# Optimization experiments

Hardware: AMD Instinct MI355X
Metric: run time of the kernel (lower is better)

## Reference

```python
import jax, jax.numpy as jnp
import numpy as np

SCALE = 1.0 / np.sqrt(128.0)  # 1/sqrt(D)


def setup_inputs() -> dict:
    key = jax.random.key(0)
    kq, kk, kv = jax.random.split(key, 3)
    B, Sq, Sk, D = 32, 2048, 2048, 128
    q = jax.random.normal(kq, (B, Sq, D), dtype=jnp.float32)
    k = jax.random.normal(kk, (B, Sk, D), dtype=jnp.float32)
    v = jax.random.normal(kv, (B, Sk, D), dtype=jnp.float32)
    return {"q": q, "k": k, "v": v}


def reference(q, k, v):
    # attention = bmm(q, k^T) * scale  -> [B, Sq, Sk]
    attention = jnp.einsum("bqd,bkd->bqk", q, k) * SCALE
    # no mask (attn_mask=None path); softmax over last dim (dim=2)
    attention = jax.nn.softmax(attention, axis=2)
    # dropout p=0.0 is identity at eval
    context = jnp.einsum("bqk,bkd->bqd", attention, v)  # [B, Sq, D]
    return (context, attention)
```

## Files before the change

kernel.cpp:

```cpp
#include <hip/hip_runtime.h>
#include <hip/hip_bf16.h>


#define B_  32
#define SQ  2048
#define SK  2048
#define DD  128
#define SCALE 0.08838834764831845f

using short8   = __attribute__((ext_vector_type(8))) short;
using ushort4t = __attribute__((ext_vector_type(4))) unsigned short;
using f32x4    = __attribute__((ext_vector_type(4))) float;

#define K_OFF 0
#define K_RS  272
#define V_OFF 8704
#define V_RS  80
#define P_OFF 18944
#define P_RS  80
#define LDS_BYTES 24064

__device__ __forceinline__ unsigned short f2bf(float f) {
  union { float f; unsigned u; } a; a.f = f;
  unsigned r = a.u + 0x7FFFu + ((a.u >> 16) & 1u);
  return (unsigned short)(r >> 16);
}

__global__ __launch_bounds__(256, 4)
void attn_fwd(const float* __restrict__ q, const float* __restrict__ k,
              const float* __restrict__ v, float* __restrict__ out) {
  __shared__ float4 smem_v[LDS_BYTES / 16];
  char* smem = (char*)smem_v;

  const int t  = threadIdx.x;
  const int w  = t >> 6;
  const int l  = t & 63;
  const int lr = l & 15;
  const int lg = l >> 4;
  const int qt = blockIdx.x;
  const int b  = blockIdx.y;
  const int q0 = qt * 64 + w * 16;

  short8 qf[4];
  {
    const float* qg = q + ((size_t)b * SQ + q0 + lr) * DD;
#pragma unroll
    for (int kk = 0; kk < 4; ++kk) {
      const int d0 = kk * 32 + lg * 8;
      float4 x = *(const float4*)(qg + d0);
      float4 y = *(const float4*)(qg + d0 + 4);
      short8 f;
      f[0] = (short)f2bf(x.x * SCALE); f[1] = (short)f2bf(x.y * SCALE);
      f[2] = (short)f2bf(x.z * SCALE); f[3] = (short)f2bf(x.w * SCALE);
      f[4] = (short)f2bf(y.x * SCALE); f[5] = (short)f2bf(y.y * SCALE);
      f[6] = (short)f2bf(y.z * SCALE); f[7] = (short)f2bf(y.w * SCALE);
      qf[kk] = f;
    }
  }

  f32x4 ctx[8];
#pragma unroll
  for (int i = 0; i < 8; ++i) ctx[i] = (f32x4){0.f, 0.f, 0.f, 0.f};
  float lsum[4] = {0.f, 0.f, 0.f, 0.f};

  char* const pl = smem + P_OFF + w * (16 * P_RS);

#pragma unroll 1
  for (int kt = 0; kt < SK / 32; ++kt) {
    const int kb = kt * 32;
    __syncthreads();
#pragma unroll
    for (int i = 0; i < 4; ++i) {
      int u = i * 256 + t;
      int row = u >> 5, c4 = u & 31;
      float4 kv = *(const float4*)(k + ((size_t)b * SK + kb + row) * DD + c4 * 4);
      ushort4t o = {f2bf(kv.x), f2bf(kv.y), f2bf(kv.z), f2bf(kv.w)};
      *(ushort4t*)(smem + K_OFF + row * K_RS + c4 * 8) = o;
    }
#pragma unroll
    for (int i = 0; i < 4; ++i) {
      int u = i * 256 + t;
      int d = u & 127, kq = u >> 7;
      const float* vp = v + ((size_t)b * SK + kb + kq * 4) * DD + d;
      ushort4t o = {f2bf(vp[0]), f2bf(vp[DD]), f2bf(vp[2 * DD]), f2bf(vp[3 * DD])};
      *(ushort4t*)(smem + V_OFF + d * V_RS + kq * 8) = o;
    }
    __syncthreads();

    f32x4 s0 = {0.f, 0.f, 0.f, 0.f}, s1 = {0.f, 0.f, 0.f, 0.f};
#pragma unroll
    for (int kk = 0; kk < 4; ++kk) {
      short8 b0 = *(const short8*)(smem + K_OFF + lr * K_RS + kk * 64 + lg * 16);
      short8 b1 = *(const short8*)(smem + K_OFF + (16 + lr) * K_RS + kk * 64 + lg * 16);
      s0 = __builtin_amdgcn_mfma_f32_16x16x32_bf16(qf[kk], b0, s0, 0, 0, 0);
      s1 = __builtin_amdgcn_mfma_f32_16x16x32_bf16(qf[kk], b1, s1, 0, 0, 0);
    }

#pragma unroll
    for (int ri = 0; ri < 4; ++ri) {
      float e0 = __expf(s0[ri]);
      float e1 = __expf(s1[ri]);
      lsum[ri] += e0 + e1;
      int prow = lg * 4 + ri;
      *(unsigned short*)(pl + prow * P_RS + lr * 2)        = f2bf(e0);
      *(unsigned short*)(pl + prow * P_RS + (16 + lr) * 2) = f2bf(e1);
    }
    short8 pa = *(const short8*)(pl + lr * P_RS + lg * 16);
#pragma unroll
    for (int nd = 0; nd < 8; ++nd) {
      short8 vb = *(const short8*)(smem + V_OFF + (nd * 16 + lr) * V_RS + lg * 16);
      ctx[nd] = __builtin_amdgcn_mfma_f32_16x16x32_bf16(pa, vb, ctx[nd], 0, 0, 0);
    }
  }

#pragma unroll
  for (int ri = 0; ri < 4; ++ri) {
#pragma unroll
    for (int off = 1; off < 16; off <<= 1)
      lsum[ri] += __shfl_xor(lsum[ri], off, 64);
  }
  float rinv[4];
#pragma unroll
  for (int ri = 0; ri < 4; ++ri) rinv[ri] = 1.0f / lsum[ri];

  {
    float* co = out + ((size_t)b * SQ + q0) * DD;
#pragma unroll
    for (int nd = 0; nd < 8; ++nd)
#pragma unroll
      for (int ri = 0; ri < 4; ++ri) {
        int row = lg * 4 + ri;
        co[(size_t)row * DD + nd * 16 + lr] = ctx[nd][ri] * rinv[ri];
      }
  }

  float* ao = out + (size_t)B_ * SQ * DD + ((size_t)b * SQ + q0) * SK;
#pragma unroll 1
  for (int kt = 0; kt < SK / 32; ++kt) {
    const int kb = kt * 32;
    __syncthreads();
#pragma unroll
    for (int i = 0; i < 4; ++i) {
      int u = i * 256 + t;
      int row = u >> 5, c4 = u & 31;
      float4 kv = *(const float4*)(k + ((size_t)b * SK + kb + row) * DD + c4 * 4);
      ushort4t o = {f2bf(kv.x), f2bf(kv.y), f2bf(kv.z), f2bf(kv.w)};
      *(ushort4t*)(smem + K_OFF + row * K_RS + c4 * 8) = o;
    }
    __syncthreads();

    f32x4 s0 = {0.f, 0.f, 0.f, 0.f}, s1 = {0.f, 0.f, 0.f, 0.f};
#pragma unroll
    for (int kk = 0; kk < 4; ++kk) {
      short8 b0 = *(const short8*)(smem + K_OFF + lr * K_RS + kk * 64 + lg * 16);
      short8 b1 = *(const short8*)(smem + K_OFF + (16 + lr) * K_RS + kk * 64 + lg * 16);
      s0 = __builtin_amdgcn_mfma_f32_16x16x32_bf16(qf[kk], b0, s0, 0, 0, 0);
      s1 = __builtin_amdgcn_mfma_f32_16x16x32_bf16(qf[kk], b1, s1, 0, 0, 0);
    }
#pragma unroll
    for (int ri = 0; ri < 4; ++ri) {
      float p0 = __expf(s0[ri]) * rinv[ri];
      float p1 = __expf(s1[ri]) * rinv[ri];
      int row = lg * 4 + ri;
      ao[(size_t)row * SK + kb + lr]      = p0;
      ao[(size_t)row * SK + kb + 16 + lr] = p1;
    }
  }
}

extern "C" void kernel_launch(void* const* d_in, const int* in_sizes, int n_in,
                              void* d_out, int out_size, void* d_ws, size_t ws_size,
                              hipStream_t stream) {
  const float* q = (const float*)d_in[0];
  const float* k = (const float*)d_in[1];
  const float* v = (const float*)d_in[2];
  float* out = (float*)d_out;
  dim3 grid(SQ / 64, B_, 1);
  attn_fwd<<<grid, 256, 0, stream>>>(q, k, v, out);
}
```

Baseline: 891.3 us.

## Precompute bf16 swizzled Q/K/V in workspace and double-buffer async LDS loads

Adds a prep kernel that converts Q (pre-scaled), K and V to bf16 once and stores K and V in a tile-major, XOR-swizzled layout in the workspace. Without it, every query block re-reads and re-converts the fp32 K and V. The main kernel now streams tiles with global_load_lds into double-buffered LDS, which overlaps loads with MFMA work and removes one barrier per iteration. It also remaps block IDs to group blocks of the same batch, widens the second pass to 64-key tiles, and stages the probability tile through LDS to issue coalesced float4 stores. The cost is an extra kernel launch, workspace traffic and more LDS use per block.

```diff
diff --git a/kernel.cpp b/kernel.cpp
--- a/kernel.cpp
+++ b/kernel.cpp
@@ -8,17 +8,15 @@
 #define DD  128
 #define SCALE 0.08838834764831845f
 
-using short8   = __attribute__((ext_vector_type(8))) short;
-using ushort4t = __attribute__((ext_vector_type(4))) unsigned short;
-using f32x4    = __attribute__((ext_vector_type(4))) float;
-
-#define K_OFF 0
-#define K_RS  272
-#define V_OFF 8704
-#define V_RS  80
-#define P_OFF 18944
-#define P_RS  80
-#define LDS_BYTES 24064
+#define WSQ_OFF 0u
+#define WSK_OFF (16u << 20)
+#define WSV_OFF (32u << 20)
+
+using short8 = __attribute__((ext_vector_type(8))) short;
+using f32x4  = __attribute__((ext_vector_type(4))) float;
+
+typedef const __attribute__((address_space(1))) unsigned int* gp_t;
+typedef __attribute__((address_space(3))) unsigned int* sp_t;
 
 __device__ __forceinline__ unsigned short f2bf(float f) {
   union { float f; unsigned u; } a; a.f = f;
@@ -26,36 +24,77 @@
   return (unsigned short)(r >> 16);
 }
 
+__device__ __forceinline__ void gl16(const char* g, char* s) {
+  __builtin_amdgcn_global_load_lds((gp_t)g, (sp_t)s, 16, 0, 0);
+}
+
+__global__ void prep(const float* __restrict__ q, const float* __restrict__ k,
+                     const float* __restrict__ v, char* __restrict__ ws) {
+  const int id = blockIdx.x;
+  const int t  = threadIdx.x;
+  if (id < 4096) {
+    size_t u = (size_t)id * 256 + t;
+    const float* src = q + u * 8;
+    float4 a = *(const float4*)src, c = *(const float4*)(src + 4);
+    short8 o;
+    o[0] = (short)f2bf(a.x * SCALE); o[1] = (short)f2bf(a.y * SCALE);
+    o[2] = (short)f2bf(a.z * SCALE); o[3] = (short)f2bf(a.w * SCALE);
+    o[4] = (short)f2bf(c.x * SCALE); o[5] = (short)f2bf(c.y * SCALE);
+    o[6] = (short)f2bf(c.z * SCALE); o[7] = (short)f2bf(c.w * SCALE);
+    *(short8*)(ws + WSQ_OFF + u * 16) = o;
+  } else if (id < 8192) {
+    size_t u = (size_t)(id - 4096) * 256 + t;
+    int c = u & 15, s = (u >> 4) & 2047, b = u >> 15;
+    const float* src = k + ((size_t)b * SQ + s) * DD + c * 8;
+    float4 a = *(const float4*)src, d = *(const float4*)(src + 4);
+    short8 o;
+    o[0] = (short)f2bf(a.x); o[1] = (short)f2bf(a.y);
+    o[2] = (short)f2bf(a.z); o[3] = (short)f2bf(a.w);
+    o[4] = (short)f2bf(d.x); o[5] = (short)f2bf(d.y);
+    o[6] = (short)f2bf(d.z); o[7] = (short)f2bf(d.w);
+    size_t idx = (size_t)(b * 64 + (s >> 5)) * 512 + (s & 31) * 16 + (c ^ (s & 7));
+    *(short8*)(ws + WSK_OFF + idx * 16) = o;
+  } else {
+    size_t u = (size_t)(id - 8192) * 256 + t;
+    int c = u & 3, d = (u >> 2) & 127, tile = (u >> 9) & 63, b = u >> 15;
+    const float* src = v + ((size_t)b * SK + tile * 32 + c * 8) * DD + d;
+    short8 o;
+#pragma unroll
+    for (int j = 0; j < 8; ++j) o[j] = (short)f2bf(src[(size_t)j * DD]);
+    size_t idx = (size_t)(b * 64 + tile) * 512 + d * 4 + (c ^ (d & 3));
+    *(short8*)(ws + WSV_OFF + idx * 16) = o;
+  }
+}
+
+#define LDS_BYTES 40960
+
 __global__ __launch_bounds__(256, 4)
-void attn_fwd(const float* __restrict__ q, const float* __restrict__ k,
-              const float* __restrict__ v, float* __restrict__ out) {
-  __shared__ float4 smem_v[LDS_BYTES / 16];
-  char* smem = (char*)smem_v;
+void attn_main(const char* __restrict__ ws, float* __restrict__ out) {
+  __shared__ __align__(16) char smem[LDS_BYTES];
 
   const int t  = threadIdx.x;
   const int w  = t >> 6;
   const int l  = t & 63;
   const int lr = l & 15;
   const int lg = l >> 4;
-  const int qt = blockIdx.x;
-  const int b  = blockIdx.y;
+
+  const int orig = blockIdx.x;
+  const int wgid = (orig & 7) * 128 + (orig >> 3);
+  const int b  = wgid >> 5;
+  const int qt = wgid & 31;
   const int q0 = qt * 64 + w * 16;
 
+  const char* wsQ = ws + WSQ_OFF;
+  const char* kt_base = ws + WSK_OFF + (size_t)(b * 64) * 8192;
+  const char* vt_base = ws + WSV_OFF + (size_t)(b * 64) * 8192;
+  char* const scr = smem + 32768 + w * 2048;
+
   short8 qf[4];
   {
-    const float* qg = q + ((size_t)b * SQ + q0 + lr) * DD;
-#pragma unroll
-    for (int kk = 0; kk < 4; ++kk) {
-      const int d0 = kk * 32 + lg * 8;
-      float4 x = *(const float4*)(qg + d0);
-      float4 y = *(const float4*)(qg + d0 + 4);
-      short8 f;
-      f[0] = (short)f2bf(x.x * SCALE); f[1] = (short)f2bf(x.y * SCALE);
-      f[2] = (short)f2bf(x.z * SCALE); f[3] = (short)f2bf(x.w * SCALE);
-      f[4] = (short)f2bf(y.x * SCALE); f[5] = (short)f2bf(y.y * SCALE);
-      f[6] = (short)f2bf(y.z * SCALE); f[7] = (short)f2bf(y.w * SCALE);
-      qf[kk] = f;
-    }
+    const char* qrow = wsQ + ((size_t)b * SQ + q0 + lr) * 256;
+#pragma unroll
+    for (int kk = 0; kk < 4; ++kk)
+      qf[kk] = *(const short8*)(qrow + kk * 64 + lg * 16);
   }
 
   f32x4 ctx[8];
@@ -63,54 +102,57 @@
   for (int i = 0; i < 8; ++i) ctx[i] = (f32x4){0.f, 0.f, 0.f, 0.f};
   float lsum[4] = {0.f, 0.f, 0.f, 0.f};
 
-  char* const pl = smem + P_OFF + w * (16 * P_RS);
+  {
+    int s0 = w * 2048;
+    gl16(kt_base + s0 + l * 16, smem + s0);
+    gl16(kt_base + s0 + 1024 + l * 16, smem + s0 + 1024);
+    gl16(vt_base + s0 + l * 16, smem + 16384 + s0);
+    gl16(vt_base + s0 + 1024 + l * 16, smem + 16384 + s0 + 1024);
+  }
+  __syncthreads();
 
 #pragma unroll 1
-  for (int kt = 0; kt < SK / 32; ++kt) {
-    const int kb = kt * 32;
+  for (int kt = 0; kt < 64; ++kt) {
+    char* kb = smem + (kt & 1) * 8192;
+    char* vb = smem + 16384 + (kt & 1) * 8192;
+    if (kt + 1 < 64) {
+      int nb = ((kt + 1) & 1) * 8192;
+      const char* ksrc = kt_base + (size_t)(kt + 1) * 8192;
+      const char* vsrc = vt_base + (size_t)(kt + 1) * 8192;
+      int s0 = w * 2048;
+      gl16(ksrc + s0 + l * 16, smem + nb + s0);
+      gl16(ksrc + s0 + 1024 + l * 16, smem + nb + s0 + 1024);
+      gl16(vsrc + s0 + l * 16, smem + 16384 + nb + s0);
+      gl16(vsrc + s0 + 1024 + l * 16, smem + 16384 + nb + s0 + 1024);
+    }
+
+    f32x4 s0v = {0.f, 0.f, 0.f, 0.f}, s1v = {0.f, 0.f, 0.f, 0.f};
+#pragma unroll
+    for (int kk = 0; kk < 4; ++kk) {
+      int cpr = (((kk * 4 + lg) ^ (lr & 7)) << 4);
+      short8 b0 = *(const short8*)(kb + lr * 256 + cpr);
+      short8 b1 = *(const short8*)(kb + 4096 + lr * 256 + cpr);
+      s0v = __builtin_amdgcn_mfma_f32_16x16x32_bf16(qf[kk], b0, s0v, 0, 0, 0);
+      s1v = __builtin_amdgcn_mfma_f32_16x16x32_bf16(qf[kk], b1, s1v, 0, 0, 0);
+    }
+
+#pragma unroll
+    for (int ri = 0; ri < 4; ++ri) {
+      float e0 = __expf(s0v[ri]);
+      float e1 = __expf(s1v[ri]);
+      lsum[ri] += e0 + e1;
+      int row = lg * 4 + ri;
+      *(unsigned short*)(scr + row * 64 + lr * 2)      = f2bf(e0);
+      *(unsigned short*)(scr + row * 64 + 32 + lr * 2) = f2bf(e1);
+    }
+    short8 pa = *(const short8*)(scr + lr * 64 + lg * 16);
+#pragma unroll
+    for (int nd = 0; nd < 8; ++nd) {
+      int d = nd * 16 + lr;
+      short8 vv = *(const short8*)(vb + ((d * 4 + (lg ^ (lr & 3))) << 4));
+      ctx[nd] = __builtin_amdgcn_mfma_f32_16x16x32_bf16(pa, vv, ctx[nd], 0, 0, 0);
+    }
     __syncthreads();
-#pragma unroll
-    for (int i = 0; i < 4; ++i) {
-      int u = i * 256 + t;
-      int row = u >> 5, c4 = u & 31;
-      float4 kv = *(const float4*)(k + ((size_t)b * SK + kb + row) * DD + c4 * 4);
-      ushort4t o = {f2bf(kv.x), f2bf(kv.y), f2bf(kv.z), f2bf(kv.w)};
-      *(ushort4t*)(smem + K_OFF + row * K_RS + c4 * 8) = o;
-    }
-#pragma unroll
-    for (int i = 0; i < 4; ++i) {
-      int u = i * 256 + t;
-      int d = u & 127, kq = u >> 7;
-      const float* vp = v + ((size_t)b * SK + kb + kq * 4) * DD + d;
-      ushort4t o = {f2bf(vp[0]), f2bf(vp[DD]), f2bf(vp[2 * DD]), f2bf(vp[3 * DD])};
-      *(ushort4t*)(smem + V_OFF + d * V_RS + kq * 8) = o;
-    }
-    __syncthreads();
-
-    f32x4 s0 = {0.f, 0.f, 0.f, 0.f}, s1 = {0.f, 0.f, 0.f, 0.f};
-#pragma unroll
-    for (int kk = 0; kk < 4; ++kk) {
-      short8 b0 = *(const short8*)(smem + K_OFF + lr * K_RS + kk * 64 + lg * 16);
-      short8 b1 = *(const short8*)(smem + K_OFF + (16 + lr) * K_RS + kk * 64 + lg * 16);
-      s0 = __builtin_amdgcn_mfma_f32_16x16x32_bf16(qf[kk], b0, s0, 0, 0, 0);
-      s1 = __builtin_amdgcn_mfma_f32_16x16x32_bf16(qf[kk], b1, s1, 0, 0, 0);
-    }
-
-#pragma unroll
-    for (int ri = 0; ri < 4; ++ri) {
-      float e0 = __expf(s0[ri]);
-      float e1 = __expf(s1[ri]);
-      lsum[ri] += e0 + e1;
-      int prow = lg * 4 + ri;
-      *(unsigned short*)(pl + prow * P_RS + lr * 2)        = f2bf(e0);
-      *(unsigned short*)(pl + prow * P_RS + (16 + lr) * 2) = f2bf(e1);
-    }
-    short8 pa = *(const short8*)(pl + lr * P_RS + lg * 16);
-#pragma unroll
-    for (int nd = 0; nd < 8; ++nd) {
-      short8 vb = *(const short8*)(smem + V_OFF + (nd * 16 + lr) * V_RS + lg * 16);
-      ctx[nd] = __builtin_amdgcn_mfma_f32_16x16x32_bf16(pa, vb, ctx[nd], 0, 0, 0);
-    }
   }
 
 #pragma unroll
@@ -135,36 +177,59 @@
   }
 
   float* ao = out + (size_t)B_ * SQ * DD + ((size_t)b * SQ + q0) * SK;
+
+  {
+    int s0 = w * 4096;
+#pragma unroll
+    for (int i = 0; i < 4; ++i)
+      gl16(kt_base + s0 + i * 1024 + l * 16, smem + s0 + i * 1024);
+  }
+  __syncthreads();
+
 #pragma unroll 1
-  for (int kt = 0; kt < SK / 32; ++kt) {
-    const int kb = kt * 32;
+  for (int t2 = 0; t2 < 32; ++t2) {
+    char* kb = smem + (t2 & 1) * 16384;
+    if (t2 + 1 < 32) {
+      int nb = ((t2 + 1) & 1) * 16384;
+      const char* ksrc = kt_base + (size_t)(t2 + 1) * 16384;
+      int s0 = w * 4096;
+#pragma unroll
+      for (int i = 0; i < 4; ++i)
+        gl16(ksrc + s0 + i * 1024 + l * 16, smem + nb + s0 + i * 1024);
+    }
+
+    f32x4 sv[4];
+#pragma unroll
+    for (int j = 0; j < 4; ++j) sv[j] = (f32x4){0.f, 0.f, 0.f, 0.f};
+#pragma unroll
+    for (int kk = 0; kk < 4; ++kk) {
+      int cpr = (((kk * 4 + lg) ^ (lr & 7)) << 4);
+#pragma unroll
+      for (int j = 0; j < 4; ++j) {
+        short8 bb = *(const short8*)(kb + (j * 16 + lr) * 256 + cpr);
+        sv[j] = __builtin_amdgcn_mfma_f32_16x16x32_bf16(qf[kk], bb, sv[j], 0, 0, 0);
+      }
+    }
+
+#pragma unroll
+    for (int h = 0; h < 2; ++h) {
+#pragma unroll
+      for (int ri = 0; ri < 4; ++ri) {
+        int row = lg * 4 + ri;
+        float p0 = __expf(sv[2 * h][ri]) * rinv[ri];
+        float p1 = __expf(sv[2 * h + 1][ri]) * rinv[ri];
+        *(float*)(scr + row * 128 + (((lr + row * 4) & 31) << 2))      = p0;
+        *(float*)(scr + row * 128 + (((16 + lr + row * 4) & 31) << 2)) = p1;
+      }
+#pragma unroll
+      for (int jj = 0; jj < 2; ++jj) {
+        int idx = l + jj * 64;
+        int row = idx >> 3, c4 = idx & 7;
+        f32x4 vv = *(const f32x4*)(scr + row * 128 + (((c4 + row) & 7) << 4));
+        *(f32x4*)(ao + (size_t)row * SK + t2 * 64 + h * 32 + c4 * 4) = vv;
+      }
+    }
     __syncthreads();
-#pragma unroll
-    for (int i = 0; i < 4; ++i) {
-      int u = i * 256 + t;
-      int row = u >> 5, c4 = u & 31;
-      float4 kv = *(const float4*)(k + ((size_t)b * SK + kb + row) * DD + c4 * 4);
-      ushort4t o = {f2bf(kv.x), f2bf(kv.y), f2bf(kv.z), f2bf(kv.w)};
-      *(ushort4t*)(smem + K_OFF + row * K_RS + c4 * 8) = o;
-    }
-    __syncthreads();
-
-    f32x4 s0 = {0.f, 0.f, 0.f, 0.f}, s1 = {0.f, 0.f, 0.f, 0.f};
-#pragma unroll
-    for (int kk = 0; kk < 4; ++kk) {
-      short8 b0 = *(const short8*)(smem + K_OFF + lr * K_RS + kk * 64 + lg * 16);
-      short8 b1 = *(const short8*)(smem + K_OFF + (16 + lr) * K_RS + kk * 64 + lg * 16);
-      s0 = __builtin_amdgcn_mfma_f32_16x16x32_bf16(qf[kk], b0, s0, 0, 0, 0);
-      s1 = __builtin_amdgcn_mfma_f32_16x16x32_bf16(qf[kk], b1, s1, 0, 0, 0);
-    }
-#pragma unroll
-    for (int ri = 0; ri < 4; ++ri) {
-      float p0 = __expf(s0[ri]) * rinv[ri];
-      float p1 = __expf(s1[ri]) * rinv[ri];
-      int row = lg * 4 + ri;
-      ao[(size_t)row * SK + kb + lr]      = p0;
-      ao[(size_t)row * SK + kb + 16 + lr] = p1;
-    }
   }
 }
 
@@ -175,6 +240,8 @@
   const float* k = (const float*)d_in[1];
   const float* v = (const float*)d_in[2];
   float* out = (float*)d_out;
-  dim3 grid(SQ / 64, B_, 1);
-  attn_fwd<<<grid, 256, 0, stream>>>(q, k, v, out);
-}
+  char* ws = (char*)d_ws;
+
+  prep<<<12288, 256, 0, stream>>>(q, k, v, ws);
+  attn_main<<<1024, 256, 0, stream>>>(ws, out);
+}
```

Result: faster. 754.4 us (-15.4%).
